# Optimization experiments

Measured on AMD Instinct MI355X. Metric: run time of the kernel, lower is better.

Reference implementation:

```python
import jax, jax.numpy as jnp
import numpy as np

N_BUS = 4096
BATCH = 1024


def setup_inputs() -> dict:
    key = jax.random.key(0)
    ks = jax.random.split(key, 10)
    u = jax.random.normal(ks[0], (BATCH, N_BUS), dtype=jnp.float32)
    w = jax.random.normal(ks[1], (BATCH, N_BUS), dtype=jnp.float32)
    # parameters (torch.rand -> uniform[0,1); Linear init ~ U(-1/sqrt(n), 1/sqrt(n)))
    G = jax.random.uniform(ks[2], (N_BUS, N_BUS), dtype=jnp.float32)
    B = jax.random.uniform(ks[3], (N_BUS, N_BUS), dtype=jnp.float32)
    bias_p = jax.random.uniform(ks[4], (1, N_BUS), dtype=jnp.float32)
    bias_q = jax.random.uniform(ks[5], (1, N_BUS), dtype=jnp.float32)
    lim = 1.0 / np.sqrt(N_BUS)
    Wp = jax.random.uniform(ks[6], (N_BUS, N_BUS), dtype=jnp.float32, minval=-lim, maxval=lim)
    bp = jax.random.uniform(ks[7], (N_BUS,), dtype=jnp.float32, minval=-lim, maxval=lim)
    Wq = jax.random.uniform(ks[8], (N_BUS, N_BUS), dtype=jnp.float32, minval=-lim, maxval=lim)
    bq = jax.random.uniform(ks[9], (N_BUS,), dtype=jnp.float32, minval=-lim, maxval=lim)
    return {"u": u, "w": w, "G": G, "B": B, "bias_p": bias_p, "bias_q": bias_q,
            "Wp": Wp, "bp": bp, "Wq": Wq, "bq": bq}


def reference(u, w, G, B, bias_p, bias_q, Wp, bp, Wq, bq):
    # Algebraically identical to the original's outer-product form:
    # p_i = sum_k (u_i u_k + w_i w_k) G_ik + (w_i u_k - u_i w_k) B_ik
    #     = u_i (G u)_i + w_i (G w)_i + w_i (B u)_i - u_i (B w)_i
    # q_i = sum_k (w_i u_k - u_i w_k) G_ik - (u_i u_k + w_i w_k) B_ik
    #     = w_i (G u)_i - u_i (G w)_i - u_i (B u)_i - w_i (B w)_i
    Gu = u @ G.T  # (batch, n_bus): (G u)_i = sum_k G_ik u_k
    Gw = w @ G.T
    Bu = u @ B.T
    Bw = w @ B.T
    p = u * Gu + w * Gw + w * Bu - u * Bw + bias_p
    q = w * Gu - u * Gw - u * Bu - w * Bw + bias_q
    # nn.Linear: y = x @ W^T + b
    p = p @ Wp.T + bp
    q = q @ Wq.T + bq
    return (p, q)
```

## Files before the change

### kernel.cpp

```cpp
#include <hip/hip_runtime.h>
#include <hip/hip_bf16.h>

#define NB 4096
#define MB 1024
#define SZ ((size_t)MB * NB)
#define NN ((size_t)NB * NB)

typedef __bf16 bf16_t;
typedef __attribute__((ext_vector_type(8))) __bf16 bf16x8;
typedef __attribute__((ext_vector_type(4))) float f32x4;
typedef __attribute__((ext_vector_type(4))) unsigned int u32x4;

#define AS1 __attribute__((address_space(1)))
#define AS3 __attribute__((address_space(3)))


__device__ __forceinline__ bf16x8 neg8(bf16x8 x) {
  u32x4 t;
  __builtin_memcpy(&t, &x, 16);
  t ^= 0x80008000u;
  bf16x8 y;
  __builtin_memcpy(&y, &t, 16);
  return y;
}

__device__ __forceinline__ bf16x8 cvt8(float4 a, float4 b) {
  bf16x8 v;
  v[0] = (bf16_t)a.x; v[1] = (bf16_t)a.y; v[2] = (bf16_t)a.z; v[3] = (bf16_t)a.w;
  v[4] = (bf16_t)b.x; v[5] = (bf16_t)b.y; v[6] = (bf16_t)b.z; v[7] = (bf16_t)b.w;
  return v;
}

#define MFMA16(a, b, c) __builtin_amdgcn_mfma_f32_16x16x32_bf16((a), (b), (c), 0, 0, 0)

#define ITEM_S (SZ / 8)
#define ITEM_N (NN / 8)

__global__ __launch_bounds__(256) void prep6_kernel(
    const float* __restrict__ u, const float* __restrict__ w,
    const float* __restrict__ G, const float* __restrict__ Bm,
    const float* __restrict__ Wp, const float* __restrict__ Wq,
    bf16_t* __restrict__ ws) {
  size_t stride = (size_t)gridDim.x * blockDim.x;
  const size_t tot = 2 * ITEM_S + 4 * ITEM_N;
  for (size_t i = (size_t)blockIdx.x * blockDim.x + threadIdx.x; i < tot;
       i += stride) {
    const float* src;
    bf16_t* dst;
    size_t off;
    if (i < ITEM_S) { src = u; dst = ws; off = i; }
    else if (i < 2 * ITEM_S) { src = w; dst = ws + SZ; off = i - ITEM_S; }
    else if (i < 2 * ITEM_S + ITEM_N) { src = G; dst = ws + 2 * SZ; off = i - 2 * ITEM_S; }
    else if (i < 2 * ITEM_S + 2 * ITEM_N) { src = Bm; dst = ws + 2 * SZ + NN; off = i - 2 * ITEM_S - ITEM_N; }
    else if (i < 2 * ITEM_S + 3 * ITEM_N) { src = Wp; dst = ws + 2 * SZ + 2 * NN; off = i - 2 * ITEM_S - 2 * ITEM_N; }
    else { src = Wq; dst = ws + 2 * SZ + 3 * NN; off = i - 2 * ITEM_S - 3 * ITEM_N; }
    const float4* s = reinterpret_cast<const float4*>(src) + off * 2;
    reinterpret_cast<bf16x8*>(dst)[off] = cvt8(s[0], s[1]);
  }
}

__global__ __launch_bounds__(256) void prep4_kernel(
    const float* __restrict__ u, const float* __restrict__ w,
    const float* __restrict__ G, const float* __restrict__ Bm,
    bf16_t* __restrict__ ws) {
  size_t stride = (size_t)gridDim.x * blockDim.x;
  const size_t tot = 2 * ITEM_S + 2 * ITEM_N;
  for (size_t i = (size_t)blockIdx.x * blockDim.x + threadIdx.x; i < tot;
       i += stride) {
    const float* src;
    bf16_t* dst;
    size_t off;
    if (i < ITEM_S) { src = u; dst = ws; off = i; }
    else if (i < 2 * ITEM_S) { src = w; dst = ws + SZ; off = i - ITEM_S; }
    else if (i < 2 * ITEM_S + ITEM_N) { src = G; dst = ws + 2 * SZ; off = i - 2 * ITEM_S; }
    else { src = Bm; dst = ws + 2 * SZ + NN; off = i - 2 * ITEM_S - ITEM_N; }
    const float4* s = reinterpret_cast<const float4*>(src) + off * 2;
    reinterpret_cast<bf16x8*>(dst)[off] = cvt8(s[0], s[1]);
  }
}

__global__ __launch_bounds__(512, 2) void fused1_v3(
    const float* __restrict__ u, const float* __restrict__ w,
    const bf16_t* __restrict__ ubf, const bf16_t* __restrict__ wbf,
    const bf16_t* __restrict__ Gbf, const bf16_t* __restrict__ Bbf,
    const float* __restrict__ bias_p, const float* __restrict__ bias_q,
    bf16_t* __restrict__ pq) {
  __shared__ bf16_t lds[2][4][128 * 64];
  const int tid = threadIdx.x, lane = tid & 63, wv = tid >> 6;
  const int bid = blockIdx.x;
  const int t = (bid & 7) * 32 + (bid >> 3);
  const int row0 = (t & 7) * 128, col0 = (t >> 3) * 128;
  const int wm = (wv >> 2) * 64, wn = (wv & 3) * 32;
  const int lr = lane & 15, kq = lane >> 4;

  const int rA = tid >> 3;
  const int kkc = (tid & 7) ^ (rA & 7);
  const bf16_t* bases[4] = {ubf, wbf, Gbf, Bbf};
  const int r0s[4] = {row0, row0, col0, col0};
  const bf16_t* gsA[4];
  const bf16_t* gsB[4];
#pragma unroll
  for (int o = 0; o < 4; ++o) {
    gsA[o] = bases[o] + (size_t)(r0s[o] + rA) * NB + kkc * 8;
    gsB[o] = gsA[o] + (size_t)64 * NB;
  }

#define F1_ST(bufv, o, ktn)                                                    \
  do {                                                                         \
    __builtin_amdgcn_global_load_lds(                                          \
        (const AS1 unsigned int*)(gsA[o] + (ktn)),                             \
        (AS3 unsigned int*)(&lds[bufv][o][wv * 512]), 16, 0, 0);               \
    __builtin_amdgcn_global_load_lds(                                          \
        (const AS1 unsigned int*)(gsB[o] + (ktn)),                             \
        (AS3 unsigned int*)(&lds[bufv][o][4096 + wv * 512]), 16, 0, 0);        \
  } while (0)

  int kread[2], aoff[4], boff[2];
#pragma unroll
  for (int ks = 0; ks < 2; ++ks) kread[ks] = ((ks * 4 + kq) ^ (lr & 7)) << 3;
#pragma unroll
  for (int m = 0; m < 4; ++m) aoff[m] = (wm + m * 16 + lr) * 64;
#pragma unroll
  for (int n = 0; n < 2; ++n) boff[n] = (wn + n * 16 + lr) * 64;

#define F1_LD(o, roff, ks) \
  (*reinterpret_cast<const bf16x8*>(&lds[cur][o][(roff) + kread[ks]]))

  f32x4 aS[4][2] = {}, aT[4][2] = {};

  {
    F1_ST(0, 0, 0); F1_ST(0, 1, 0); F1_ST(0, 2, 0); F1_ST(0, 3, 0);
    asm volatile("s_waitcnt vmcnt(0)" ::: "memory");
  }
  __syncthreads();

  const int NIT = NB / 64;
  for (int it = 0; it < NIT; ++it) {
    const int cur = it & 1;
    const int nxt = cur ^ 1;
    const bool pf = (it + 1) < NIT;
    const int ktn = (it + 1) * 64;
#pragma unroll
    for (int ks = 0; ks < 2; ++ks) {
      bf16x8 bG[2], bB[2], bBn[2];
#pragma unroll
      for (int mh = 0; mh < 2; ++mh) {
        if (mh == 0) {
          bG[0] = F1_LD(2, boff[0], ks);
          bG[1] = F1_LD(2, boff[1], ks);
          bB[0] = F1_LD(3, boff[0], ks);
          bB[1] = F1_LD(3, boff[1], ks);
          bBn[0] = neg8(bB[0]);
          bBn[1] = neg8(bB[1]);
        }
        bf16x8 au2[2], aw2[2];
#pragma unroll
        for (int i = 0; i < 2; ++i) {
          au2[i] = F1_LD(0, aoff[2 * mh + i], ks);
          aw2[i] = F1_LD(1, aoff[2 * mh + i], ks);
        }
        if (ks == 0 && pf) {
          if (mh == 0) { F1_ST(nxt, 0, ktn); F1_ST(nxt, 1, ktn); }
          else         { F1_ST(nxt, 2, ktn); F1_ST(nxt, 3, ktn); }
        }
        __builtin_amdgcn_s_barrier();
        __builtin_amdgcn_sched_barrier(0);
        __builtin_amdgcn_s_setprio(1);
#pragma unroll
        for (int i = 0; i < 2; ++i) {
          const int m = 2 * mh + i;
#pragma unroll
          for (int n = 0; n < 2; ++n) {
            aS[m][n] = MFMA16(au2[i], bG[n], aS[m][n]);
            aS[m][n] = MFMA16(aw2[i], bBn[n], aS[m][n]);
            aT[m][n] = MFMA16(aw2[i], bG[n], aT[m][n]);
            aT[m][n] = MFMA16(au2[i], bB[n], aT[m][n]);
          }
        }
        __builtin_amdgcn_s_setprio(0);
        __builtin_amdgcn_sched_barrier(0);
        if (ks == 1 && mh == 1)
          asm volatile("s_waitcnt vmcnt(0)" ::: "memory");
        __builtin_amdgcn_s_barrier();
        __builtin_amdgcn_sched_barrier(0);
      }
    }
  }

  const int fr = lane & 15, fq = kq;
#pragma unroll
  for (int m = 0; m < 4; ++m)
#pragma unroll
    for (int n = 0; n < 2; ++n)
#pragma unroll
      for (int j = 0; j < 4; ++j) {
        int r = row0 + wm + m * 16 + fq * 4 + j;
        int c = col0 + wn + n * 16 + fr;
        size_t idx = (size_t)r * NB + c;
        float U = u[idx], W = w[idx];
        float S = aS[m][n][j], T = aT[m][n][j];
        pq[idx] = (bf16_t)(U * S + W * T + bias_p[c]);
        pq[SZ + idx] = (bf16_t)(W * S - U * T + bias_q[c]);
      }
}

__global__ __launch_bounds__(512, 2) void gemm2_v4(
    const bf16_t* __restrict__ pq, const bf16_t* __restrict__ Wpb,
    const bf16_t* __restrict__ Wqb, const float* __restrict__ bp,
    const float* __restrict__ bq, float* __restrict__ out) {
  __shared__ bf16_t lA[2][128 * 64];
  __shared__ bf16_t lW[2][256 * 64];
  const int tid = threadIdx.x, lane = tid & 63, wv = tid >> 6;
  const int bid = blockIdx.x;
  const int t = (bid & 7) * 32 + (bid >> 3);
  const int z = t >> 7;
  const int s = t & 127;
  const int row0 = (s & 7) * 128, col0 = (s >> 3) * 256;

  const bf16_t* A = pq + (size_t)z * SZ;
  const bf16_t* Wm = z ? Wqb : Wpb;
  const float* bias = z ? bq : bp;
  float* C = out + (size_t)z * SZ;

  const int wm = (wv >> 2) * 64, wn = (wv & 3) * 64;
  const int lr = lane & 15, kq = lane >> 4;

  const int rA = tid >> 3;
  const int kkc = (tid & 7) ^ (rA & 7);
  const bf16_t* gA_[2];
  const bf16_t* gW_[4];
#pragma unroll
  for (int j = 0; j < 2; ++j)
    gA_[j] = A + (size_t)(row0 + rA + 64 * j) * NB + kkc * 8;
#pragma unroll
  for (int j = 0; j < 4; ++j)
    gW_[j] = Wm + (size_t)(col0 + rA + 64 * j) * NB + kkc * 8;

#define G2_STA(bufv, j, ktn)                                                   \
  __builtin_amdgcn_global_load_lds(                                            \
      (const AS1 unsigned int*)(gA_[j] + (ktn)),                               \
      (AS3 unsigned int*)(&lA[bufv][(j) * 4096 + wv * 512]), 16, 0, 0)
#define G2_STW(bufv, j, ktn)                                                   \
  __builtin_amdgcn_global_load_lds(                                            \
      (const AS1 unsigned int*)(gW_[j] + (ktn)),                               \
      (AS3 unsigned int*)(&lW[bufv][(j) * 4096 + wv * 512]), 16, 0, 0)

  int kread[2], aoff[4], boff[4];
#pragma unroll
  for (int ks = 0; ks < 2; ++ks) kread[ks] = ((ks * 4 + kq) ^ (lr & 7)) << 3;
#pragma unroll
  for (int m = 0; m < 4; ++m) aoff[m] = (wm + m * 16 + lr) * 64;
#pragma unroll
  for (int n = 0; n < 4; ++n) boff[n] = (wn + n * 16 + lr) * 64;

  f32x4 acc[4][4] = {};

  {
    G2_STA(0, 0, 0); G2_STA(0, 1, 0);
    G2_STW(0, 0, 0); G2_STW(0, 1, 0); G2_STW(0, 2, 0); G2_STW(0, 3, 0);
    asm volatile("s_waitcnt vmcnt(0)" ::: "memory");
  }
  __syncthreads();

  const int NIT = NB / 64;
  for (int it = 0; it < NIT; ++it) {
    const int cur = it & 1;
    const int nxt = cur ^ 1;
    const bool pf = (it + 1) < NIT;
    const int ktn = (it + 1) * 64;
#pragma unroll
    for (int ks = 0; ks < 2; ++ks) {
      bf16x8 bw[4];
#pragma unroll
      for (int mh = 0; mh < 2; ++mh) {
        if (mh == 0) {
#pragma unroll
          for (int n = 0; n < 4; ++n)
            bw[n] = *reinterpret_cast<const bf16x8*>(
                &lW[cur][boff[n] + kread[ks]]);
        }
        bf16x8 au2[2];
#pragma unroll
        for (int i = 0; i < 2; ++i)
          au2[i] = *reinterpret_cast<const bf16x8*>(
              &lA[cur][aoff[2 * mh + i] + kread[ks]]);
        if (pf) {
          const int ph = ks * 2 + mh;
          if (ph == 0) { G2_STA(nxt, 0, ktn); G2_STA(nxt, 1, ktn); }
          else if (ph == 1) { G2_STW(nxt, 0, ktn); G2_STW(nxt, 1, ktn); }
          else if (ph == 2) { G2_STW(nxt, 2, ktn); G2_STW(nxt, 3, ktn); }
        }
        __builtin_amdgcn_s_barrier();
        __builtin_amdgcn_sched_barrier(0);
        __builtin_amdgcn_s_setprio(1);
#pragma unroll
        for (int i = 0; i < 2; ++i) {
          const int m = 2 * mh + i;
#pragma unroll
          for (int n = 0; n < 4; ++n)
            acc[m][n] = MFMA16(au2[i], bw[n], acc[m][n]);
        }
        __builtin_amdgcn_s_setprio(0);
        __builtin_amdgcn_sched_barrier(0);
        if (ks == 1 && mh == 1)
          asm volatile("s_waitcnt vmcnt(0)" ::: "memory");
        __builtin_amdgcn_s_barrier();
        __builtin_amdgcn_sched_barrier(0);
      }
    }
  }

  const int fr = lane & 15, fq = kq;
#pragma unroll
  for (int m = 0; m < 4; ++m)
#pragma unroll
    for (int n = 0; n < 4; ++n)
#pragma unroll
      for (int j = 0; j < 4; ++j) {
        int r = row0 + wm + m * 16 + fq * 4 + j;
        int c = col0 + wn + n * 16 + fr;
        C[(size_t)r * NB + c] = acc[m][n][j] + bias[c];
      }
}

__device__ __forceinline__ int swz_off32(int r, int kk) {
  return r * 32 + ((kk ^ ((r >> 1) & 3)) << 3);
}

__device__ __forceinline__ void fb_stage_f32(const float* __restrict__ src,
                                             int row0, int k0, bf16_t* lds, int t) {
  int r = t >> 2, kk = t & 3;
  const float* p = src + (size_t)(row0 + r) * NB + k0 + (kk << 3);
  float4 v0 = *reinterpret_cast<const float4*>(p);
  float4 v1 = *reinterpret_cast<const float4*>(p + 4);
  *reinterpret_cast<bf16x8*>(lds + swz_off32(r, kk)) = cvt8(v0, v1);
}

__global__ __launch_bounds__(256, 2) void fb_gemm2(
    const bf16_t* __restrict__ pq, const float* __restrict__ Wp,
    const float* __restrict__ Wq, const float* __restrict__ bp,
    const float* __restrict__ bq, float* __restrict__ out) {
  __shared__ bf16_t lA[128 * 32], lW[128 * 32];
  const int z = blockIdx.z;
  const bf16_t* A = pq + (size_t)z * SZ;
  const float* Wm = z ? Wq : Wp;
  const float* bias = z ? bq : bp;
  float* C = out + (size_t)z * SZ;
  const int tid = threadIdx.x;
  const int lane = tid & 63, wv = tid >> 6;
  const int wm = (wv >> 1) * 64, wn = (wv & 1) * 64;
  const int row0 = blockIdx.y * 128, col0 = blockIdx.x * 128;
  const int lr = lane & 15, kq = lane >> 4;
  const int fslot = (kq ^ ((lr >> 1) & 3)) << 3;
  f32x4 acc[4][4] = {};
  for (int kt = 0; kt < NB; kt += 32) {
#pragma unroll
    for (int p = 0; p < 2; ++p) {
      int cb = p * 256 + wv * 64;
      int ci = cb + lane;
      int r = ci >> 2, kl = ci & 3;
      int ks = kl ^ ((r >> 1) & 3);
      const bf16_t* g = A + (size_t)(row0 + r) * NB + kt + (ks << 3);
      __builtin_amdgcn_global_load_lds((const AS1 unsigned int*)g,
                                       (AS3 unsigned int*)(lA + cb * 8), 16, 0, 0);
    }
#pragma unroll
    for (int p = 0; p < 2; ++p)
      fb_stage_f32(Wm, col0, kt, lW, p * 256 + tid);
    __syncthreads();
    bf16x8 af[4], bg[4];
#pragma unroll
    for (int m = 0; m < 4; ++m)
      af[m] = *reinterpret_cast<const bf16x8*>(lA + (wm + m * 16 + lr) * 32 + fslot);
#pragma unroll
    for (int n = 0; n < 4; ++n)
      bg[n] = *reinterpret_cast<const bf16x8*>(lW + (wn + n * 16 + lr) * 32 + fslot);
#pragma unroll
    for (int m = 0; m < 4; ++m)
#pragma unroll
      for (int n = 0; n < 4; ++n)
        acc[m][n] = MFMA16(af[m], bg[n], acc[m][n]);
    __syncthreads();
  }
  const int fr = lane & 15, fq = lane >> 4;
#pragma unroll
  for (int m = 0; m < 4; ++m)
#pragma unroll
    for (int n = 0; n < 4; ++n)
#pragma unroll
      for (int j = 0; j < 4; ++j) {
        int r = row0 + wm + m * 16 + fq * 4 + j;
        int c = col0 + wn + n * 16 + fr;
        C[(size_t)r * NB + c] = acc[m][n][j] + bias[c];
      }
}

__global__ __launch_bounds__(512, 2) void fb_fused1(
    const float* __restrict__ u, const float* __restrict__ w,
    const float* __restrict__ G, const float* __restrict__ Bm,
    const float* __restrict__ bias_p, const float* __restrict__ bias_q,
    bf16_t* __restrict__ pq) {
  __shared__ bf16_t lU[128 * 32], lW[128 * 32], lG[128 * 32], lB[128 * 32];
  const int tid = threadIdx.x;
  const int lane = tid & 63, wv = tid >> 6;
  const int wm = (wv >> 2) * 64, wn = (wv & 3) * 32;
  const int row0 = blockIdx.y * 128, col0 = blockIdx.x * 128;
  const int lr = lane & 15, kq = lane >> 4;
  const int fslot = (kq ^ ((lr >> 1) & 3)) << 3;
  f32x4 aS[4][2] = {}, aT[4][2] = {};
  for (int kt = 0; kt < NB; kt += 32) {
    fb_stage_f32(u, row0, kt, lU, tid);
    fb_stage_f32(w, row0, kt, lW, tid);
    fb_stage_f32(G, col0, kt, lG, tid);
    fb_stage_f32(Bm, col0, kt, lB, tid);
    __syncthreads();
    bf16x8 au[4], aw[4], bG[2], bB[2], bBn[2];
#pragma unroll
    for (int m = 0; m < 4; ++m) {
      int off = (wm + m * 16 + lr) * 32 + fslot;
      au[m] = *reinterpret_cast<const bf16x8*>(lU + off);
      aw[m] = *reinterpret_cast<const bf16x8*>(lW + off);
    }
#pragma unroll
    for (int n = 0; n < 2; ++n) {
      int off = (wn + n * 16 + lr) * 32 + fslot;
      bG[n] = *reinterpret_cast<const bf16x8*>(lG + off);
      bB[n] = *reinterpret_cast<const bf16x8*>(lB + off);
      bBn[n] = neg8(bB[n]);
    }
#pragma unroll
    for (int m = 0; m < 4; ++m)
#pragma unroll
      for (int n = 0; n < 2; ++n) {
        aS[m][n] = MFMA16(au[m], bG[n], aS[m][n]);
        aS[m][n] = MFMA16(aw[m], bBn[n], aS[m][n]);
        aT[m][n] = MFMA16(aw[m], bG[n], aT[m][n]);
        aT[m][n] = MFMA16(au[m], bB[n], aT[m][n]);
      }
    __syncthreads();
  }
  const int fr = lane & 15, fq = lane >> 4;
#pragma unroll
  for (int m = 0; m < 4; ++m)
#pragma unroll
    for (int n = 0; n < 2; ++n)
#pragma unroll
      for (int j = 0; j < 4; ++j) {
        int r = row0 + wm + m * 16 + fq * 4 + j;
        int c = col0 + wn + n * 16 + fr;
        size_t idx = (size_t)r * NB + c;
        float U = u[idx], W = w[idx];
        float S = aS[m][n][j], T = aT[m][n][j];
        pq[idx] = (bf16_t)(U * S + W * T + bias_p[c]);
        pq[SZ + idx] = (bf16_t)(W * S - U * T + bias_q[c]);
      }
}

extern "C" void kernel_launch(void* const* d_in, const int* in_sizes, int n_in,
                              void* d_out, int out_size, void* d_ws, size_t ws_size,
                              hipStream_t stream) {
  const float* u = (const float*)d_in[0];
  const float* w = (const float*)d_in[1];
  const float* G = (const float*)d_in[2];
  const float* Bm = (const float*)d_in[3];
  const float* bias_p = (const float*)d_in[4];
  const float* bias_q = (const float*)d_in[5];
  const float* Wp = (const float*)d_in[6];
  const float* bp = (const float*)d_in[7];
  const float* Wq = (const float*)d_in[8];
  const float* bq = (const float*)d_in[9];
  (void)in_sizes; (void)n_in; (void)out_size;

  const size_t need_full = (6 * SZ + 4 * NN) * sizeof(bf16_t);
  const size_t need_mid = (6 * SZ + 2 * NN) * sizeof(bf16_t);

  if (ws_size >= need_full) {
    bf16_t* ws = (bf16_t*)d_ws;
    bf16_t* ubf = ws;
    bf16_t* wbf = ws + SZ;
    bf16_t* Gbf = ws + 2 * SZ;
    bf16_t* Bbf = Gbf + NN;
    bf16_t* Wpb = Bbf + NN;
    bf16_t* Wqb = Wpb + NN;
    bf16_t* pqw = Wqb + NN;
    prep6_kernel<<<2048, 256, 0, stream>>>(u, w, G, Bm, Wp, Wq, ws);
    fused1_v3<<<256, 512, 0, stream>>>(u, w, ubf, wbf, Gbf, Bbf,
                                       bias_p, bias_q, pqw);
    gemm2_v4<<<256, 512, 0, stream>>>(pqw, Wpb, Wqb, bp, bq, (float*)d_out);
  } else if (ws_size >= need_mid) {
    bf16_t* ws = (bf16_t*)d_ws;
    bf16_t* ubf = ws;
    bf16_t* wbf = ws + SZ;
    bf16_t* Gbf = ws + 2 * SZ;
    bf16_t* Bbf = Gbf + NN;
    bf16_t* pqw = Bbf + NN;
    prep4_kernel<<<2048, 256, 0, stream>>>(u, w, G, Bm, ws);
    fused1_v3<<<256, 512, 0, stream>>>(u, w, ubf, wbf, Gbf, Bbf,
                                       bias_p, bias_q, pqw);
    fb_gemm2<<<dim3(NB / 128, MB / 128, 2), 256, 0, stream>>>(
        pqw, Wp, Wq, bp, bq, (float*)d_out);
  } else {
    bf16_t* pqw = (bf16_t*)d_ws;
    fb_fused1<<<dim3(NB / 128, MB / 128), 512, 0, stream>>>(
        u, w, G, Bm, bias_p, bias_q, pqw);
    fb_gemm2<<<dim3(NB / 128, MB / 128, 2), 256, 0, stream>>>(
        pqw, Wp, Wq, bp, bq, (float*)d_out);
  }
}
```

Baseline: 340.8 us.

## Deepen GEMM pipelines to four-stage K=32 LDS ring with 3-ahead prefetch

Both the fused first GEMM and the second GEMM change from a two-buffer, K=64 per stage double-buffering scheme to a four-slot ring of K=32 stages. Loads are issued three stages ahead, and waits use partial vmcnt counts instead of draining to zero. The goal is to keep more global-to-LDS traffic in flight and hide memory latency behind the MFMAs. In exchange, each stage needs more barriers, and the swizzle layout changes to match the narrower 32-element rows.

```diff
diff --git a/kernel.cpp b/kernel.cpp
--- a/kernel.cpp
+++ b/kernel.cpp
@@ -13,6 +13,12 @@
 
 #define AS1 __attribute__((address_space(1)))
 #define AS3 __attribute__((address_space(3)))
+#define GLOAD16(gp, lp)                                                        \
+  __builtin_amdgcn_global_load_lds((const AS1 unsigned int*)(gp),              \
+                                   (AS3 unsigned int*)(lp), 16, 0, 0)
+#define SBAR() __builtin_amdgcn_s_barrier()
+#define SCHEDB() __builtin_amdgcn_sched_barrier(0)
+#define MFMA16(a, b, c) __builtin_amdgcn_mfma_f32_16x16x32_bf16((a), (b), (c), 0, 0, 0)
 
 
 __device__ __forceinline__ bf16x8 neg8(bf16x8 x) {
@@ -30,8 +36,6 @@
   v[4] = (bf16_t)b.x; v[5] = (bf16_t)b.y; v[6] = (bf16_t)b.z; v[7] = (bf16_t)b.w;
   return v;
 }
-
-#define MFMA16(a, b, c) __builtin_amdgcn_mfma_f32_16x16x32_bf16((a), (b), (c), 0, 0, 0)
 
 #define ITEM_S (SZ / 8)
 #define ITEM_N (NN / 8)
@@ -79,112 +83,118 @@
   }
 }
 
-__global__ __launch_bounds__(512, 2) void fused1_v3(
+__global__ __launch_bounds__(512, 2) void fused1_v4(
     const float* __restrict__ u, const float* __restrict__ w,
     const bf16_t* __restrict__ ubf, const bf16_t* __restrict__ wbf,
     const bf16_t* __restrict__ Gbf, const bf16_t* __restrict__ Bbf,
     const float* __restrict__ bias_p, const float* __restrict__ bias_q,
     bf16_t* __restrict__ pq) {
-  __shared__ bf16_t lds[2][4][128 * 64];
+  __shared__ bf16_t lds[4][4][128 * 32];
   const int tid = threadIdx.x, lane = tid & 63, wv = tid >> 6;
   const int bid = blockIdx.x;
   const int t = (bid & 7) * 32 + (bid >> 3);
   const int row0 = (t & 7) * 128, col0 = (t >> 3) * 128;
   const int wm = (wv >> 2) * 64, wn = (wv & 3) * 32;
   const int lr = lane & 15, kq = lane >> 4;
-
-  const int rA = tid >> 3;
-  const int kkc = (tid & 7) ^ (rA & 7);
-  const bf16_t* bases[4] = {ubf, wbf, Gbf, Bbf};
-  const int r0s[4] = {row0, row0, col0, col0};
-  const bf16_t* gsA[4];
-  const bf16_t* gsB[4];
-#pragma unroll
-  for (int o = 0; o < 4; ++o) {
-    gsA[o] = bases[o] + (size_t)(r0s[o] + rA) * NB + kkc * 8;
-    gsB[o] = gsA[o] + (size_t)64 * NB;
-  }
-
-#define F1_ST(bufv, o, ktn)                                                    \
-  do {                                                                         \
-    __builtin_amdgcn_global_load_lds(                                          \
-        (const AS1 unsigned int*)(gsA[o] + (ktn)),                             \
-        (AS3 unsigned int*)(&lds[bufv][o][wv * 512]), 16, 0, 0);               \
-    __builtin_amdgcn_global_load_lds(                                          \
-        (const AS1 unsigned int*)(gsB[o] + (ktn)),                             \
-        (AS3 unsigned int*)(&lds[bufv][o][4096 + wv * 512]), 16, 0, 0);        \
-  } while (0)
-
-  int kread[2], aoff[4], boff[2];
-#pragma unroll
-  for (int ks = 0; ks < 2; ++ks) kread[ks] = ((ks * 4 + kq) ^ (lr & 7)) << 3;
-#pragma unroll
-  for (int m = 0; m < 4; ++m) aoff[m] = (wm + m * 16 + lr) * 64;
-#pragma unroll
-  for (int n = 0; n < 2; ++n) boff[n] = (wn + n * 16 + lr) * 64;
-
-#define F1_LD(o, roff, ks) \
-  (*reinterpret_cast<const bf16x8*>(&lds[cur][o][(roff) + kread[ks]]))
+  const int kswz = (kq ^ (lr & 3)) << 3;
+
+  const int srow = wv * 16 + (lane >> 2);
+  const int sc = (lane & 3) ^ ((lane >> 2) & 3);
+  const bf16_t* gsrc[4];
+  gsrc[0] = ubf + (size_t)(row0 + srow) * NB + sc * 8;
+  gsrc[1] = wbf + (size_t)(row0 + srow) * NB + sc * 8;
+  gsrc[2] = Gbf + (size_t)(col0 + srow) * NB + sc * 8;
+  gsrc[3] = Bbf + (size_t)(col0 + srow) * NB + sc * 8;
+
+#define F1_ISS(op, sl, ko) GLOAD16(gsrc[op] + (ko), &lds[sl][op][wv * 512])
+
+  int aoff[4], boff[2];
+#pragma unroll
+  for (int m = 0; m < 4; ++m) aoff[m] = (wm + m * 16 + lr) * 32 + kswz;
+#pragma unroll
+  for (int n = 0; n < 2; ++n) boff[n] = (wn + n * 16 + lr) * 32 + kswz;
 
   f32x4 aS[4][2] = {}, aT[4][2] = {};
 
-  {
-    F1_ST(0, 0, 0); F1_ST(0, 1, 0); F1_ST(0, 2, 0); F1_ST(0, 3, 0);
-    asm volatile("s_waitcnt vmcnt(0)" ::: "memory");
-  }
-  __syncthreads();
-
-  const int NIT = NB / 64;
-  for (int it = 0; it < NIT; ++it) {
-    const int cur = it & 1;
-    const int nxt = cur ^ 1;
-    const bool pf = (it + 1) < NIT;
-    const int ktn = (it + 1) * 64;
-#pragma unroll
-    for (int ks = 0; ks < 2; ++ks) {
-      bf16x8 bG[2], bB[2], bBn[2];
-#pragma unroll
-      for (int mh = 0; mh < 2; ++mh) {
-        if (mh == 0) {
-          bG[0] = F1_LD(2, boff[0], ks);
-          bG[1] = F1_LD(2, boff[1], ks);
-          bB[0] = F1_LD(3, boff[0], ks);
-          bB[1] = F1_LD(3, boff[1], ks);
-          bBn[0] = neg8(bB[0]);
-          bBn[1] = neg8(bB[1]);
-        }
-        bf16x8 au2[2], aw2[2];
-#pragma unroll
-        for (int i = 0; i < 2; ++i) {
-          au2[i] = F1_LD(0, aoff[2 * mh + i], ks);
-          aw2[i] = F1_LD(1, aoff[2 * mh + i], ks);
-        }
-        if (ks == 0 && pf) {
-          if (mh == 0) { F1_ST(nxt, 0, ktn); F1_ST(nxt, 1, ktn); }
-          else         { F1_ST(nxt, 2, ktn); F1_ST(nxt, 3, ktn); }
-        }
-        __builtin_amdgcn_s_barrier();
-        __builtin_amdgcn_sched_barrier(0);
-        __builtin_amdgcn_s_setprio(1);
-#pragma unroll
-        for (int i = 0; i < 2; ++i) {
-          const int m = 2 * mh + i;
-#pragma unroll
-          for (int n = 0; n < 2; ++n) {
-            aS[m][n] = MFMA16(au2[i], bG[n], aS[m][n]);
-            aS[m][n] = MFMA16(aw2[i], bBn[n], aS[m][n]);
-            aT[m][n] = MFMA16(aw2[i], bG[n], aT[m][n]);
-            aT[m][n] = MFMA16(au2[i], bB[n], aT[m][n]);
-          }
-        }
-        __builtin_amdgcn_s_setprio(0);
-        __builtin_amdgcn_sched_barrier(0);
-        if (ks == 1 && mh == 1)
-          asm volatile("s_waitcnt vmcnt(0)" ::: "memory");
-        __builtin_amdgcn_s_barrier();
-        __builtin_amdgcn_sched_barrier(0);
-      }
-    }
+#pragma unroll
+  for (int hh = 0; hh < 3; ++hh) {
+    F1_ISS(0, hh, hh * 32);
+    F1_ISS(1, hh, hh * 32);
+    F1_ISS(2, hh, hh * 32);
+    F1_ISS(3, hh, hh * 32);
+  }
+  asm volatile("s_waitcnt vmcnt(8)" ::: "memory");
+  SBAR();
+  SCHEDB();
+
+  const int HTOT = 2 * (NB / 64);
+  for (int h = 0; h < HTOT; ++h) {
+    const int slot = h & 3;
+    const bool pf = (h + 3) < HTOT;
+    const int pslot = (h + 3) & 3;
+    const int pko = (h + 3) * 32;
+
+    bf16x8 bG[2], bB[2], bBn[2], au2[2], aw2[2];
+#pragma unroll
+    for (int n = 0; n < 2; ++n) {
+      bG[n] = *reinterpret_cast<const bf16x8*>(&lds[slot][2][boff[n]]);
+      bB[n] = *reinterpret_cast<const bf16x8*>(&lds[slot][3][boff[n]]);
+    }
+    bBn[0] = neg8(bB[0]);
+    bBn[1] = neg8(bB[1]);
+#pragma unroll
+    for (int i = 0; i < 2; ++i) {
+      au2[i] = *reinterpret_cast<const bf16x8*>(&lds[slot][0][aoff[i]]);
+      aw2[i] = *reinterpret_cast<const bf16x8*>(&lds[slot][1][aoff[i]]);
+    }
+    if (pf) { F1_ISS(0, pslot, pko); F1_ISS(1, pslot, pko); }
+    SBAR();
+    SCHEDB();
+    __builtin_amdgcn_s_setprio(1);
+#pragma unroll
+    for (int i = 0; i < 2; ++i)
+#pragma unroll
+      for (int n = 0; n < 2; ++n) {
+        aS[i][n] = MFMA16(au2[i], bG[n], aS[i][n]);
+        aS[i][n] = MFMA16(aw2[i], bBn[n], aS[i][n]);
+        aT[i][n] = MFMA16(aw2[i], bG[n], aT[i][n]);
+        aT[i][n] = MFMA16(au2[i], bB[n], aT[i][n]);
+      }
+    __builtin_amdgcn_s_setprio(0);
+    SCHEDB();
+    SBAR();
+    SCHEDB();
+
+#pragma unroll
+    for (int i = 0; i < 2; ++i) {
+      au2[i] = *reinterpret_cast<const bf16x8*>(&lds[slot][0][aoff[2 + i]]);
+      aw2[i] = *reinterpret_cast<const bf16x8*>(&lds[slot][1][aoff[2 + i]]);
+    }
+    if (pf) { F1_ISS(2, pslot, pko); F1_ISS(3, pslot, pko); }
+    SBAR();
+    SCHEDB();
+    __builtin_amdgcn_s_setprio(1);
+#pragma unroll
+    for (int i = 0; i < 2; ++i) {
+      const int m = 2 + i;
+#pragma unroll
+      for (int n = 0; n < 2; ++n) {
+        aS[m][n] = MFMA16(au2[i], bG[n], aS[m][n]);
+        aS[m][n] = MFMA16(aw2[i], bBn[n], aS[m][n]);
+        aT[m][n] = MFMA16(aw2[i], bG[n], aT[m][n]);
+        aT[m][n] = MFMA16(au2[i], bB[n], aT[m][n]);
+      }
+    }
+    __builtin_amdgcn_s_setprio(0);
+    SCHEDB();
+    if (h < HTOT - 3)
+      asm volatile("s_waitcnt vmcnt(8)" ::: "memory");
+    else if (h == HTOT - 3)
+      asm volatile("s_waitcnt vmcnt(4)" ::: "memory");
+    else if (h == HTOT - 2)
+      asm volatile("s_waitcnt vmcnt(0)" ::: "memory");
+    SBAR();
+    SCHEDB();
   }
 
   const int fr = lane & 15, fq = kq;
@@ -204,12 +214,12 @@
       }
 }
 
-__global__ __launch_bounds__(512, 2) void gemm2_v4(
+__global__ __launch_bounds__(512, 2) void gemm2_v5(
     const bf16_t* __restrict__ pq, const bf16_t* __restrict__ Wpb,
     const bf16_t* __restrict__ Wqb, const float* __restrict__ bp,
     const float* __restrict__ bq, float* __restrict__ out) {
-  __shared__ bf16_t lA[2][128 * 64];
-  __shared__ bf16_t lW[2][256 * 64];
+  __shared__ bf16_t lA[4][128 * 32];
+  __shared__ bf16_t lW[4][256 * 32];
   const int tid = threadIdx.x, lane = tid & 63, wv = tid >> 6;
   const int bid = blockIdx.x;
   const int t = (bid & 7) * 32 + (bid >> 3);
@@ -224,90 +234,68 @@
 
   const int wm = (wv >> 2) * 64, wn = (wv & 3) * 64;
   const int lr = lane & 15, kq = lane >> 4;
-
-  const int rA = tid >> 3;
-  const int kkc = (tid & 7) ^ (rA & 7);
-  const bf16_t* gA_[2];
-  const bf16_t* gW_[4];
-#pragma unroll
-  for (int j = 0; j < 2; ++j)
-    gA_[j] = A + (size_t)(row0 + rA + 64 * j) * NB + kkc * 8;
-#pragma unroll
-  for (int j = 0; j < 4; ++j)
-    gW_[j] = Wm + (size_t)(col0 + rA + 64 * j) * NB + kkc * 8;
-
-#define G2_STA(bufv, j, ktn)                                                   \
-  __builtin_amdgcn_global_load_lds(                                            \
-      (const AS1 unsigned int*)(gA_[j] + (ktn)),                               \
-      (AS3 unsigned int*)(&lA[bufv][(j) * 4096 + wv * 512]), 16, 0, 0)
-#define G2_STW(bufv, j, ktn)                                                   \
-  __builtin_amdgcn_global_load_lds(                                            \
-      (const AS1 unsigned int*)(gW_[j] + (ktn)),                               \
-      (AS3 unsigned int*)(&lW[bufv][(j) * 4096 + wv * 512]), 16, 0, 0)
-
-  int kread[2], aoff[4], boff[4];
-#pragma unroll
-  for (int ks = 0; ks < 2; ++ks) kread[ks] = ((ks * 4 + kq) ^ (lr & 7)) << 3;
-#pragma unroll
-  for (int m = 0; m < 4; ++m) aoff[m] = (wm + m * 16 + lr) * 64;
-#pragma unroll
-  for (int n = 0; n < 4; ++n) boff[n] = (wn + n * 16 + lr) * 64;
+  const int kswz = (kq ^ (lr & 3)) << 3;
+
+  const int srow = lane >> 2;
+  const int sc = (lane & 3) ^ ((lane >> 2) & 3);
+  const bf16_t* gA0 = A + (size_t)(row0 + wv * 16 + srow) * NB + sc * 8;
+  const bf16_t* gW0 = Wm + (size_t)(col0 + wv * 32 + srow) * NB + sc * 8;
+  const bf16_t* gW1 = gW0 + (size_t)16 * NB;
+
+#define G2_ISS(sl, ko)                                                         \
+  do {                                                                         \
+    GLOAD16(gA0 + (ko), &lA[sl][wv * 512]);                                    \
+    GLOAD16(gW0 + (ko), &lW[sl][wv * 1024]);                                   \
+    GLOAD16(gW1 + (ko), &lW[sl][wv * 1024 + 512]);                             \
+  } while (0)
+
+  int aoff[4], woff[4];
+#pragma unroll
+  for (int m = 0; m < 4; ++m) aoff[m] = (wm + m * 16 + lr) * 32 + kswz;
+#pragma unroll
+  for (int n = 0; n < 4; ++n) woff[n] = (wn + n * 16 + lr) * 32 + kswz;
 
   f32x4 acc[4][4] = {};
 
-  {
-    G2_STA(0, 0, 0); G2_STA(0, 1, 0);
-    G2_STW(0, 0, 0); G2_STW(0, 1, 0); G2_STW(0, 2, 0); G2_STW(0, 3, 0);
-    asm volatile("s_waitcnt vmcnt(0)" ::: "memory");
-  }
-  __syncthreads();
-
-  const int NIT = NB / 64;
-  for (int it = 0; it < NIT; ++it) {
-    const int cur = it & 1;
-    const int nxt = cur ^ 1;
-    const bool pf = (it + 1) < NIT;
-    const int ktn = (it + 1) * 64;
-#pragma unroll
-    for (int ks = 0; ks < 2; ++ks) {
-      bf16x8 bw[4];
-#pragma unroll
-      for (int mh = 0; mh < 2; ++mh) {
-        if (mh == 0) {
-#pragma unroll
-          for (int n = 0; n < 4; ++n)
-            bw[n] = *reinterpret_cast<const bf16x8*>(
-                &lW[cur][boff[n] + kread[ks]]);
-        }
-        bf16x8 au2[2];
-#pragma unroll
-        for (int i = 0; i < 2; ++i)
-          au2[i] = *reinterpret_cast<const bf16x8*>(
-              &lA[cur][aoff[2 * mh + i] + kread[ks]]);
-        if (pf) {
-          const int ph = ks * 2 + mh;
-          if (ph == 0) { G2_STA(nxt, 0, ktn); G2_STA(nxt, 1, ktn); }
-          else if (ph == 1) { G2_STW(nxt, 0, ktn); G2_STW(nxt, 1, ktn); }
-          else if (ph == 2) { G2_STW(nxt, 2, ktn); G2_STW(nxt, 3, ktn); }
-        }
-        __builtin_amdgcn_s_barrier();
-        __builtin_amdgcn_sched_barrier(0);
-        __builtin_amdgcn_s_setprio(1);
-#pragma unroll
-        for (int i = 0; i < 2; ++i) {
-          const int m = 2 * mh + i;
-#pragma unroll
-          for (int n = 0; n < 4; ++n)
-            acc[m][n] = MFMA16(au2[i], bw[n], acc[m][n]);
-        }
-        __builtin_amdgcn_s_setprio(0);
-        __builtin_amdgcn_sched_barrier(0);
-        if (ks == 1 && mh == 1)
-          asm volatile("s_waitcnt vmcnt(0)" ::: "memory");
-        __builtin_amdgcn_s_barrier();
-        __builtin_amdgcn_sched_barrier(0);
-      }
-    }
+#pragma unroll
+  for (int hh = 0; hh < 3; ++hh) G2_ISS(hh, hh * 32);
+  asm volatile("s_waitcnt vmcnt(6)" ::: "memory");
+  SBAR();
+  SCHEDB();
+
+  const int HTOT = 2 * (NB / 64);
+  for (int h = 0; h < HTOT; ++h) {
+    const int slot = h & 3;
+    const bool pf = (h + 3) < HTOT;
+    const int pslot = (h + 3) & 3;
+    const int pko = (h + 3) * 32;
+
+    bf16x8 av[4], bw[4];
+#pragma unroll
+    for (int m = 0; m < 4; ++m)
+      av[m] = *reinterpret_cast<const bf16x8*>(&lA[slot][aoff[m]]);
+#pragma unroll
+    for (int n = 0; n < 4; ++n)
+      bw[n] = *reinterpret_cast<const bf16x8*>(&lW[slot][woff[n]]);
+    if (pf) G2_ISS(pslot, pko);
+    SBAR();
+    SCHEDB();
+    __builtin_amdgcn_s_setprio(1);
+#pragma unroll
+    for (int m = 0; m < 4; ++m)
+#pragma unroll
+      for (int n = 0; n < 4; ++n)
+        acc[m][n] = MFMA16(av[m], bw[n], acc[m][n]);
+    __builtin_amdgcn_s_setprio(0);
+    SCHEDB();
+    if (h < HTOT - 3)
+      asm volatile("s_waitcnt vmcnt(6)" ::: "memory");
+    else if (h == HTOT - 3)
+      asm volatile("s_waitcnt vmcnt(3)" ::: "memory");
+    else if (h == HTOT - 2)
+      asm volatile("s_waitcnt vmcnt(0)" ::: "memory");
+    SBAR();
+    SCHEDB();
   }
 
   const int fr = lane & 15, fq = kq;
@@ -361,8 +349,7 @@
       int r = ci >> 2, kl = ci & 3;
       int ks = kl ^ ((r >> 1) & 3);
       const bf16_t* g = A + (size_t)(row0 + r) * NB + kt + (ks << 3);
-      __builtin_amdgcn_global_load_lds((const AS1 unsigned int*)g,
-                                       (AS3 unsigned int*)(lA + cb * 8), 16, 0, 0);
+      GLOAD16(g, lA + cb * 8);
     }
 #pragma unroll
     for (int p = 0; p < 2; ++p)
@@ -484,9 +471,9 @@
     bf16_t* Wqb = Wpb + NN;
     bf16_t* pqw = Wqb + NN;
     prep6_kernel<<<2048, 256, 0, stream>>>(u, w, G, Bm, Wp, Wq, ws);
-    fused1_v3<<<256, 512, 0, stream>>>(u, w, ubf, wbf, Gbf, Bbf,
+    fused1_v4<<<256, 512, 0, stream>>>(u, w, ubf, wbf, Gbf, Bbf,
                                        bias_p, bias_q, pqw);
-    gemm2_v4<<<256, 512, 0, stream>>>(pqw, Wpb, Wqb, bp, bq, (float*)d_out);
+    gemm2_v5<<<256, 512, 0, stream>>>(pqw, Wpb, Wqb, bp, bq, (float*)d_out);
   } else if (ws_size >= need_mid) {
     bf16_t* ws = (bf16_t*)d_ws;
     bf16_t* ubf = ws;
@@ -495,7 +482,7 @@
     bf16_t* Bbf = Gbf + NN;
     bf16_t* pqw = Bbf + NN;
     prep4_kernel<<<2048, 256, 0, stream>>>(u, w, G, Bm, ws);
-    fused1_v3<<<256, 512, 0, stream>>>(u, w, ubf, wbf, Gbf, Bbf,
+    fused1_v4<<<256, 512, 0, stream>>>(u, w, ubf, wbf, Gbf, Bbf,
                                        bias_p, bias_q, pqw);
     fb_gemm2<<<dim3(NB / 128, MB / 128, 2), 256, 0, stream>>>(
         pqw, Wp, Wq, bp, bq, (float*)d_out);
```

New measurement: 320.7 us. -5.9%, faster.

## Rewrite second GEMM as 128x128 tiles with 4-stage K=32 ring pipeline

Applied to the files above, without the earlier changes.

Replaces the 512-thread 128x256-tile double-buffered second GEMM with a 256-thread 128x128-tile kernel that stages K=32 slices into a 4-slot LDS ring, keeping three loads in flight and using a single barrier per step with graded vmcnt waits. Grid doubles to 512 blocks to improve CU fill and latency hiding. Smaller tiles lower arithmetic intensity and increase global/L2 traffic for the weight matrices. Also adds helper macros as cleanup.

```diff
diff --git a/kernel.cpp b/kernel.cpp
--- a/kernel.cpp
+++ b/kernel.cpp
@@ -13,7 +13,14 @@
 
 #define AS1 __attribute__((address_space(1)))
 #define AS3 __attribute__((address_space(3)))
-
+#define GLOAD16(gp, lp)                                                        \
+  __builtin_amdgcn_global_load_lds((const AS1 unsigned int*)(gp),              \
+                                   (AS3 unsigned int*)(lp), 16, 0, 0)
+#define SBAR() __builtin_amdgcn_s_barrier()
+#define SCHEDB() __builtin_amdgcn_sched_barrier(0)
+#define MFMA16(a, b, c) __builtin_amdgcn_mfma_f32_16x16x32_bf16((a), (b), (c), 0, 0, 0)
+#define VMCNT4() asm volatile("s_waitcnt vmcnt(4)" ::: "memory")
+#define VMCNT0() asm volatile("s_waitcnt vmcnt(0)" ::: "memory")
 
 __device__ __forceinline__ bf16x8 neg8(bf16x8 x) {
   u32x4 t;
@@ -30,8 +37,6 @@
   v[4] = (bf16_t)b.x; v[5] = (bf16_t)b.y; v[6] = (bf16_t)b.z; v[7] = (bf16_t)b.w;
   return v;
 }
-
-#define MFMA16(a, b, c) __builtin_amdgcn_mfma_f32_16x16x32_bf16((a), (b), (c), 0, 0, 0)
 
 #define ITEM_S (SZ / 8)
 #define ITEM_N (NN / 8)
@@ -107,12 +112,8 @@
 
 #define F1_ST(bufv, o, ktn)                                                    \
   do {                                                                         \
-    __builtin_amdgcn_global_load_lds(                                          \
-        (const AS1 unsigned int*)(gsA[o] + (ktn)),                             \
-        (AS3 unsigned int*)(&lds[bufv][o][wv * 512]), 16, 0, 0);               \
-    __builtin_amdgcn_global_load_lds(                                          \
-        (const AS1 unsigned int*)(gsB[o] + (ktn)),                             \
-        (AS3 unsigned int*)(&lds[bufv][o][4096 + wv * 512]), 16, 0, 0);        \
+    GLOAD16(gsA[o] + (ktn), &lds[bufv][o][wv * 512]);                          \
+    GLOAD16(gsB[o] + (ktn), &lds[bufv][o][4096 + wv * 512]);                   \
   } while (0)
 
   int kread[2], aoff[4], boff[2];
@@ -130,7 +131,7 @@
 
   {
     F1_ST(0, 0, 0); F1_ST(0, 1, 0); F1_ST(0, 2, 0); F1_ST(0, 3, 0);
-    asm volatile("s_waitcnt vmcnt(0)" ::: "memory");
+    VMCNT0();
   }
   __syncthreads();
 
@@ -163,8 +164,8 @@
           if (mh == 0) { F1_ST(nxt, 0, ktn); F1_ST(nxt, 1, ktn); }
           else         { F1_ST(nxt, 2, ktn); F1_ST(nxt, 3, ktn); }
         }
-        __builtin_amdgcn_s_barrier();
-        __builtin_amdgcn_sched_barrier(0);
+        SBAR();
+        SCHEDB();
         __builtin_amdgcn_s_setprio(1);
 #pragma unroll
         for (int i = 0; i < 2; ++i) {
@@ -178,11 +179,10 @@
           }
         }
         __builtin_amdgcn_s_setprio(0);
-        __builtin_amdgcn_sched_barrier(0);
-        if (ks == 1 && mh == 1)
-          asm volatile("s_waitcnt vmcnt(0)" ::: "memory");
-        __builtin_amdgcn_s_barrier();
-        __builtin_amdgcn_sched_barrier(0);
+        SCHEDB();
+        if (ks == 1 && mh == 1) VMCNT0();
+        SBAR();
+        SCHEDB();
       }
     }
   }
@@ -204,110 +204,83 @@
       }
 }
 
-__global__ __launch_bounds__(512, 2) void gemm2_v4(
+__global__ __launch_bounds__(256, 2) void gemm2_v9(
     const bf16_t* __restrict__ pq, const bf16_t* __restrict__ Wpb,
     const bf16_t* __restrict__ Wqb, const float* __restrict__ bp,
     const float* __restrict__ bq, float* __restrict__ out) {
-  __shared__ bf16_t lA[2][128 * 64];
-  __shared__ bf16_t lW[2][256 * 64];
+  __shared__ bf16_t lds[4][2][128 * 32];
   const int tid = threadIdx.x, lane = tid & 63, wv = tid >> 6;
   const int bid = blockIdx.x;
-  const int t = (bid & 7) * 32 + (bid >> 3);
-  const int z = t >> 7;
-  const int s = t & 127;
-  const int row0 = (s & 7) * 128, col0 = (s >> 3) * 256;
+  const int t = (bid & 7) * 64 + (bid >> 3);
+  const int z = t >> 8;
+  const int s = t & 255;
+  const int row0 = (s & 7) * 128, col0 = (s >> 3) * 128;
 
   const bf16_t* A = pq + (size_t)z * SZ;
   const bf16_t* Wm = z ? Wqb : Wpb;
   const float* bias = z ? bq : bp;
   float* C = out + (size_t)z * SZ;
 
-  const int wm = (wv >> 2) * 64, wn = (wv & 3) * 64;
+  const int wm = (wv >> 1) * 64, wn = (wv & 1) * 64;
   const int lr = lane & 15, kq = lane >> 4;
-
-  const int rA = tid >> 3;
-  const int kkc = (tid & 7) ^ (rA & 7);
-  const bf16_t* gA_[2];
-  const bf16_t* gW_[4];
-#pragma unroll
-  for (int j = 0; j < 2; ++j)
-    gA_[j] = A + (size_t)(row0 + rA + 64 * j) * NB + kkc * 8;
-#pragma unroll
-  for (int j = 0; j < 4; ++j)
-    gW_[j] = Wm + (size_t)(col0 + rA + 64 * j) * NB + kkc * 8;
-
-#define G2_STA(bufv, j, ktn)                                                   \
-  __builtin_amdgcn_global_load_lds(                                            \
-      (const AS1 unsigned int*)(gA_[j] + (ktn)),                               \
-      (AS3 unsigned int*)(&lA[bufv][(j) * 4096 + wv * 512]), 16, 0, 0)
-#define G2_STW(bufv, j, ktn)                                                   \
-  __builtin_amdgcn_global_load_lds(                                            \
-      (const AS1 unsigned int*)(gW_[j] + (ktn)),                               \
-      (AS3 unsigned int*)(&lW[bufv][(j) * 4096 + wv * 512]), 16, 0, 0)
-
-  int kread[2], aoff[4], boff[4];
-#pragma unroll
-  for (int ks = 0; ks < 2; ++ks) kread[ks] = ((ks * 4 + kq) ^ (lr & 7)) << 3;
-#pragma unroll
-  for (int m = 0; m < 4; ++m) aoff[m] = (wm + m * 16 + lr) * 64;
-#pragma unroll
-  for (int n = 0; n < 4; ++n) boff[n] = (wn + n * 16 + lr) * 64;
+  const int kswz = (kq ^ ((lr >> 1) & 3)) << 3;
+
+  const int srow = tid >> 2;
+  const int sc = (tid & 3) ^ ((tid >> 3) & 3);
+  const bf16_t* gA0 = A + (size_t)(row0 + srow) * NB + sc * 8;
+  const bf16_t* gA1 = gA0 + (size_t)64 * NB;
+  const bf16_t* gW0 = Wm + (size_t)(col0 + srow) * NB + sc * 8;
+  const bf16_t* gW1 = gW0 + (size_t)64 * NB;
+
+#define G2_ISSUE(hh)                                                           \
+  do {                                                                         \
+    const int _sl = (hh) & 3;                                                  \
+    const int _ko = (hh) * 32;                                                 \
+    GLOAD16(gA0 + _ko, &lds[_sl][0][wv * 512]);                                \
+    GLOAD16(gA1 + _ko, &lds[_sl][0][2048 + wv * 512]);                         \
+    GLOAD16(gW0 + _ko, &lds[_sl][1][wv * 512]);                                \
+    GLOAD16(gW1 + _ko, &lds[_sl][1][2048 + wv * 512]);                         \
+  } while (0)
+
+  int aoff[4], woff[4];
+#pragma unroll
+  for (int m = 0; m < 4; ++m) aoff[m] = (wm + m * 16 + lr) * 32 + kswz;
+#pragma unroll
+  for (int n = 0; n < 4; ++n) woff[n] = (wn + n * 16 + lr) * 32 + kswz;
 
   f32x4 acc[4][4] = {};
 
-  {
-    G2_STA(0, 0, 0); G2_STA(0, 1, 0);
-    G2_STW(0, 0, 0); G2_STW(0, 1, 0); G2_STW(0, 2, 0); G2_STW(0, 3, 0);
-    asm volatile("s_waitcnt vmcnt(0)" ::: "memory");
-  }
-  __syncthreads();
-
-  const int NIT = NB / 64;
-  for (int it = 0; it < NIT; ++it) {
-    const int cur = it & 1;
-    const int nxt = cur ^ 1;
-    const bool pf = (it + 1) < NIT;
-    const int ktn = (it + 1) * 64;
-#pragma unroll
-    for (int ks = 0; ks < 2; ++ks) {
-      bf16x8 bw[4];
-#pragma unroll
-      for (int mh = 0; mh < 2; ++mh) {
-        if (mh == 0) {
-#pragma unroll
-          for (int n = 0; n < 4; ++n)
-            bw[n] = *reinterpret_cast<const bf16x8*>(
-                &lW[cur][boff[n] + kread[ks]]);
-        }
-        bf16x8 au2[2];
-#pragma unroll
-        for (int i = 0; i < 2; ++i)
-          au2[i] = *reinterpret_cast<const bf16x8*>(
-              &lA[cur][aoff[2 * mh + i] + kread[ks]]);
-        if (pf) {
-          const int ph = ks * 2 + mh;
-          if (ph == 0) { G2_STA(nxt, 0, ktn); G2_STA(nxt, 1, ktn); }
-          else if (ph == 1) { G2_STW(nxt, 0, ktn); G2_STW(nxt, 1, ktn); }
-          else if (ph == 2) { G2_STW(nxt, 2, ktn); G2_STW(nxt, 3, ktn); }
-        }
-        __builtin_amdgcn_s_barrier();
-        __builtin_amdgcn_sched_barrier(0);
-        __builtin_amdgcn_s_setprio(1);
-#pragma unroll
-        for (int i = 0; i < 2; ++i) {
-          const int m = 2 * mh + i;
-#pragma unroll
-          for (int n = 0; n < 4; ++n)
-            acc[m][n] = MFMA16(au2[i], bw[n], acc[m][n]);
-        }
-        __builtin_amdgcn_s_setprio(0);
-        __builtin_amdgcn_sched_barrier(0);
-        if (ks == 1 && mh == 1)
-          asm volatile("s_waitcnt vmcnt(0)" ::: "memory");
-        __builtin_amdgcn_s_barrier();
-        __builtin_amdgcn_sched_barrier(0);
-      }
-    }
+  G2_ISSUE(0); G2_ISSUE(1); G2_ISSUE(2);
+  VMCNT4();
+  SBAR();
+  SCHEDB();
+
+  const int HTOT = 2 * (NB / 64);
+  for (int h = 0; h < HTOT; ++h) {
+    const int slot = h & 3;
+    const bool pf = (h + 3) < HTOT;
+
+    bf16x8 av[4], bw[4];
+#pragma unroll
+    for (int m = 0; m < 4; ++m)
+      av[m] = *reinterpret_cast<const bf16x8*>(&lds[slot][0][aoff[m]]);
+#pragma unroll
+    for (int n = 0; n < 4; ++n)
+      bw[n] = *reinterpret_cast<const bf16x8*>(&lds[slot][1][woff[n]]);
+    if (pf) G2_ISSUE(h + 3);
+#pragma unroll
+    for (int m = 0; m < 4; ++m)
+#pragma unroll
+      for (int n = 0; n < 4; ++n)
+        acc[m][n] = MFMA16(av[m], bw[n], acc[m][n]);
+    if (h < HTOT - 3)
+      VMCNT4();
+    else if (h == HTOT - 3)
+      asm volatile("s_waitcnt vmcnt(2)" ::: "memory");
+    else if (h == HTOT - 2)
+      VMCNT0();
+    SBAR();
+    SCHEDB();
   }
 
   const int fr = lane & 15, fq = kq;
@@ -361,8 +334,7 @@
       int r = ci >> 2, kl = ci & 3;
       int ks = kl ^ ((r >> 1) & 3);
       const bf16_t* g = A + (size_t)(row0 + r) * NB + kt + (ks << 3);
-      __builtin_amdgcn_global_load_lds((const AS1 unsigned int*)g,
-                                       (AS3 unsigned int*)(lA + cb * 8), 16, 0, 0);
+      GLOAD16(g, lA + cb * 8);
     }
 #pragma unroll
     for (int p = 0; p < 2; ++p)
@@ -486,7 +458,7 @@
     prep6_kernel<<<2048, 256, 0, stream>>>(u, w, G, Bm, Wp, Wq, ws);
     fused1_v3<<<256, 512, 0, stream>>>(u, w, ubf, wbf, Gbf, Bbf,
                                        bias_p, bias_q, pqw);
-    gemm2_v4<<<256, 512, 0, stream>>>(pqw, Wpb, Wqb, bp, bq, (float*)d_out);
+    gemm2_v9<<<512, 256, 0, stream>>>(pqw, Wpb, Wqb, bp, bq, (float*)d_out);
   } else if (ws_size >= need_mid) {
     bf16_t* ws = (bf16_t*)d_ws;
     bf16_t* ubf = ws;
```

Result: faster. 302.5 us (-11.2%).
